# Performance work log

Measured on AMD Instinct MI355X. Metric: run time of the kernel, lower is better.

The kernel has to match this reference:

```python
import jax, jax.numpy as jnp
import numpy as np

EPS = 1e-8


def setup_inputs() -> dict:
    key = jax.random.key(0)
    k1, k2, k3, k4, k5 = jax.random.split(key, 5)
    N, B, T, D = 8, 2, 2048, 2048
    F = 4 * D
    blocks = jax.random.normal(k1, (N, B, T, D), dtype=jnp.float32)
    partial_block = jax.random.normal(k2, (B, T, D), dtype=jnp.float32)
    proj_w = jax.random.normal(k3, (D,), dtype=jnp.float32) * 0.02
    norm_scale = jnp.ones((D,), dtype=jnp.float32)
    ffn_w1 = jax.random.normal(k4, (D, F), dtype=jnp.float32) * 0.02
    ffn_w2 = jax.random.normal(k5, (F, D), dtype=jnp.float32) * 0.02
    return {
        "blocks": blocks,
        "partial_block": partial_block,
        "proj_w": proj_w,
        "norm_scale": norm_scale,
        "ffn_w1": ffn_w1,
        "ffn_w2": ffn_w2,
    }


def reference(blocks, partial_block, proj_w, norm_scale, ffn_w1, ffn_w2):
    # Stack completed blocks with current partial sum: V [N1, B, T, D]
    V = jnp.concatenate([blocks, partial_block[None]], axis=0)
    # RMSNorm over D (keys)
    rms = jnp.sqrt(jnp.mean(V * V, axis=-1, keepdims=True) + EPS)
    K = norm_scale * V / rms
    # Pseudo-query dot-product logits [N1, B, T], softmax over blocks (axis 0)
    logits = jnp.einsum('nbtd,d->nbt', K, proj_w)
    alpha = jax.nn.softmax(logits, axis=0)
    # Weighted sum of raw values -> new hidden state h [B, T, D]
    h = jnp.einsum('nbt,nbtd->btd', alpha, V)
    # Sublayer: standard FFN (D -> 4D gelu -> D)
    f_out = jax.nn.gelu(h @ ffn_w1) @ ffn_w2
    # layer_number % block_size != 0 branch: accumulate partial sum
    new_partial = partial_block + f_out
    return h, new_partial
```

## Files before the change

### kernel.cpp

```cpp
#include <hip/hip_runtime.h>

typedef unsigned short ushort_t;
typedef __bf16 bf16x8 __attribute__((ext_vector_type(8)));
typedef float f32x4 __attribute__((ext_vector_type(4)));

#define NB 8
#define BB 2
#define TT 2048
#define DD 2048
#define FF 8192
#define MM (BB * TT)
#define BTD ((size_t)BB * TT * DD)

__device__ __forceinline__ unsigned short f2bf(float f) {
  unsigned int u = __float_as_uint(f);
  u += 0x7FFFu + ((u >> 16) & 1u);
  return (unsigned short)(u >> 16);
}

__device__ __forceinline__ float gelu_tanh(float x) {
  float u = 0.7978845608028654f * (x + 0.044715f * x * x * x);
  float e = __expf(2.0f * u);
  float th = 1.0f - 2.0f / (e + 1.0f);
  return 0.5f * x * (1.0f + th);
}

template <int N>
__device__ __forceinline__ void wait_vmcnt() {
  if constexpr (N == 0) asm volatile("s_waitcnt vmcnt(0)" ::: "memory");
  else if constexpr (N == 2) asm volatile("s_waitcnt vmcnt(2)" ::: "memory");
  else if constexpr (N == 4) asm volatile("s_waitcnt vmcnt(4)" ::: "memory");
  else if constexpr (N == 6) asm volatile("s_waitcnt vmcnt(6)" ::: "memory");
}

#define ASYNC_COPY16(gp, lp)                                                   \
  __builtin_amdgcn_global_load_lds(                                            \
      (__attribute__((address_space(1))) void*)(gp),                           \
      (__attribute__((address_space(3))) void*)(lp), 16, 0, 0)

__global__ __launch_bounds__(256) void transpose_conv(
    const float* __restrict__ in, ushort_t* __restrict__ out, int R, int C) {
  __shared__ float tile[32][33];
  const int tx = threadIdx.x & 31, ty = threadIdx.x >> 5;
  const int r0 = blockIdx.y * 32, c0 = blockIdx.x * 32;
#pragma unroll
  for (int i = 0; i < 32; i += 8)
    tile[ty + i][tx] = in[(size_t)(r0 + ty + i) * C + (c0 + tx)];
  __syncthreads();
#pragma unroll
  for (int i = 0; i < 32; i += 8)
    out[(size_t)(c0 + ty + i) * R + (r0 + tx)] = f2bf(tile[tx][ty + i]);
}

__global__ __launch_bounds__(256) void attn_fuse(
    const float* __restrict__ blocks, const float* __restrict__ partial,
    const float* __restrict__ proj_w, const float* __restrict__ norm_scale,
    float* __restrict__ h_out, ushort_t* __restrict__ h_bf) {
  const int t = threadIdx.x;
  const int bt = blockIdx.x;
  const size_t rowoff = (size_t)bt * DD;
  const int d0 = t * 4;

  float w[8];
  {
    float4 ns = *(const float4*)(norm_scale + d0);
    float4 pw = *(const float4*)(proj_w + d0);
    w[0] = ns.x * pw.x; w[1] = ns.y * pw.y; w[2] = ns.z * pw.z; w[3] = ns.w * pw.w;
    ns = *(const float4*)(norm_scale + 1024 + d0);
    pw = *(const float4*)(proj_w + 1024 + d0);
    w[4] = ns.x * pw.x; w[5] = ns.y * pw.y; w[6] = ns.z * pw.z; w[7] = ns.w * pw.w;
  }

  float ss[9], dt[9];
#pragma unroll
  for (int n = 0; n < 9; ++n) {
    const float* rp = (n < 8) ? (blocks + (size_t)n * BTD + rowoff)
                              : (partial + rowoff);
    float4 v0 = *(const float4*)(rp + d0);
    float4 v1 = *(const float4*)(rp + 1024 + d0);
    ss[n] = v0.x * v0.x + v0.y * v0.y + v0.z * v0.z + v0.w * v0.w +
            v1.x * v1.x + v1.y * v1.y + v1.z * v1.z + v1.w * v1.w;
    dt[n] = v0.x * w[0] + v0.y * w[1] + v0.z * w[2] + v0.w * w[3] +
            v1.x * w[4] + v1.y * w[5] + v1.z * w[6] + v1.w * w[7];
  }

  __shared__ float red[2][9][4];
  const int lane = t & 63, wv = t >> 6;
#pragma unroll
  for (int n = 0; n < 9; ++n) {
    float a = ss[n], c = dt[n];
#pragma unroll
    for (int off = 32; off > 0; off >>= 1) {
      a += __shfl_down(a, off, 64);
      c += __shfl_down(c, off, 64);
    }
    if (lane == 0) { red[0][n][wv] = a; red[1][n][wv] = c; }
  }
  __syncthreads();
  __shared__ float logit_s[9];
  if (t < 9) {
    float a = red[0][t][0] + red[0][t][1] + red[0][t][2] + red[0][t][3];
    float c = red[1][t][0] + red[1][t][1] + red[1][t][2] + red[1][t][3];
    logit_s[t] = c * rsqrtf(a * (1.0f / (float)DD) + 1e-8f);
  }
  __syncthreads();

  float lg[9], mx = -1e30f;
#pragma unroll
  for (int n = 0; n < 9; ++n) { lg[n] = logit_s[n]; mx = fmaxf(mx, lg[n]); }
  float den = 0.0f;
#pragma unroll
  for (int n = 0; n < 9; ++n) { lg[n] = __expf(lg[n] - mx); den += lg[n]; }
  const float inv = 1.0f / den;

  float h[8] = {0, 0, 0, 0, 0, 0, 0, 0};
#pragma unroll
  for (int n = 0; n < 9; ++n) {
    const float* rp = (n < 8) ? (blocks + (size_t)n * BTD + rowoff)
                              : (partial + rowoff);
    float4 v0 = *(const float4*)(rp + d0);
    float4 v1 = *(const float4*)(rp + 1024 + d0);
    const float a = lg[n] * inv;
    h[0] += a * v0.x; h[1] += a * v0.y; h[2] += a * v0.z; h[3] += a * v0.w;
    h[4] += a * v1.x; h[5] += a * v1.y; h[6] += a * v1.z; h[7] += a * v1.w;
  }

  float4 o0 = {h[0], h[1], h[2], h[3]}, o1 = {h[4], h[5], h[6], h[7]};
  *(float4*)(h_out + rowoff + d0) = o0;
  *(float4*)(h_out + rowoff + 1024 + d0) = o1;
  uint2 p0, p1;
  p0.x = (unsigned)f2bf(h[0]) | ((unsigned)f2bf(h[1]) << 16);
  p0.y = (unsigned)f2bf(h[2]) | ((unsigned)f2bf(h[3]) << 16);
  p1.x = (unsigned)f2bf(h[4]) | ((unsigned)f2bf(h[5]) << 16);
  p1.y = (unsigned)f2bf(h[6]) | ((unsigned)f2bf(h[7]) << 16);
  *(uint2*)(h_bf + rowoff + d0) = p0;
  *(uint2*)(h_bf + rowoff + 1024 + d0) = p1;
}

template <int BN, int EPI>
__global__ __launch_bounds__(512) void gemm256(
    const ushort_t* __restrict__ A, const ushort_t* __restrict__ BT,
    const int K, const int N, const int GX, ushort_t* __restrict__ Cb,
    const float* __restrict__ addend, float* __restrict__ Cf) {
  constexpr int BM = 256;
  constexpr int WCN = BN / 4;
  constexpr int MF = 8;
  constexpr int NF = WCN / 16;
  constexpr int NH = NF / 2;
  constexpr int NCB = BN / 64;
  constexpr int AUS = BM * 64;
  constexpr int WP2 = (BN == 256) ? 6 : 4;

  __shared__ __align__(16) ushort_t lds0[(BM + BN) * 64];
  __shared__ __align__(16) ushort_t lds1[(BM + BN) * 64];

  const int t = threadIdx.x;
  const int lane = t & 63, wv = t >> 6;
  const int wr = wv >> 2, wc = wv & 3;
  const int fr = lane & 15;

  const int nwg = gridDim.x;
  const int wg = blockIdx.x;
  const int swz = (wg & 7) * (nwg >> 3) + (wg >> 3);
  const int bx = swz % GX, by = swz / GX;
  const int row0 = by * BM, col0 = bx * BN;

  const int sr = t >> 3;
  const int scolb = ((t & 7) * 16) ^ ((sr & 7) << 4);
  const ushort_t* gA = A + (size_t)(row0 + sr) * K + (scolb >> 1);
  const ushort_t* gB = BT + (size_t)(col0 + sr) * K + (scolb >> 1);

#define STAGE_A(W, c, KT)                                                      \
  ASYNC_COPY16(gA + (size_t)((c)*64) * K + (KT)*64, &W[(c)*4096 + wv * 512])
#define STAGE_B(W, c, KT)                                                      \
  ASYNC_COPY16(gB + (size_t)((c)*64) * K + (KT)*64,                            \
               &W[AUS + (c)*4096 + wv * 512])

  const int s_lane = (fr & 7) << 4;
  const int offk0 = ((lane >> 4) * 16) ^ s_lane;
  const int offk1 = (64 + (lane >> 4) * 16) ^ s_lane;
  const int aoffA = (wr * 128 + fr) * 128;
  int boffB[NF];
#pragma unroll
  for (int n = 0; n < NF; ++n)
    boffB[n] = AUS * 2 + (wc * WCN + n * 16 + fr) * 128;

  f32x4 acc[MF][NF];
#pragma unroll
  for (int m = 0; m < MF; ++m)
#pragma unroll
    for (int n = 0; n < NF; ++n) {
      f32x4 z = {0.f, 0.f, 0.f, 0.f};
      acc[m][n] = z;
    }

#define MFMA_(a, b, c) __builtin_amdgcn_mfma_f32_16x16x32_bf16(a, b, c, 0, 0, 0)

#define TILE(Rb, Wb, KT, S)                                                    \
  {                                                                            \
    const char* _L = (const char*)Rb;                                          \
    bf16x8 af[4][2], b0[NH][2], b1[NH][2];                                     \
                                                 \
    _Pragma("unroll") for (int m = 0; m < 4; ++m) {                            \
      af[m][0] = *(const bf16x8*)(_L + aoffA + m * 2048 + offk0);              \
      af[m][1] = *(const bf16x8*)(_L + aoffA + m * 2048 + offk1);              \
    }                                                                          \
    _Pragma("unroll") for (int n = 0; n < NH; ++n) {                           \
      b0[n][0] = *(const bf16x8*)(_L + boffB[n] + offk0);                      \
      b0[n][1] = *(const bf16x8*)(_L + boffB[n] + offk1);                      \
    }                                                                          \
    if (S) {                                                                   \
      STAGE_A(Wb, 0, KT); STAGE_A(Wb, 2, KT);                                  \
      STAGE_B(Wb, 0, KT); STAGE_B(Wb, 1, KT);                                  \
    }                                                                          \
    __builtin_amdgcn_s_barrier();                                              \
    __builtin_amdgcn_s_setprio(1);                                             \
    _Pragma("unroll") for (int m = 0; m < 4; ++m)                              \
      _Pragma("unroll") for (int n = 0; n < NH; ++n) {                         \
        acc[m][n] = MFMA_(af[m][0], b0[n][0], acc[m][n]);                      \
        acc[m][n] = MFMA_(af[m][1], b0[n][1], acc[m][n]);                      \
      }                                                                        \
    __builtin_amdgcn_s_setprio(0);                                             \
    __builtin_amdgcn_s_barrier();                                              \
                                                 \
    _Pragma("unroll") for (int n = 0; n < NH; ++n) {                           \
      b1[n][0] = *(const bf16x8*)(_L + boffB[NH + n] + offk0);                 \
      b1[n][1] = *(const bf16x8*)(_L + boffB[NH + n] + offk1);                 \
    }                                                                          \
    if (S && BN == 256) { STAGE_B(Wb, 2, KT); STAGE_B(Wb, 3, KT); }            \
    __builtin_amdgcn_s_barrier();                                              \
    __builtin_amdgcn_s_setprio(1);                                             \
    _Pragma("unroll") for (int m = 0; m < 4; ++m)                              \
      _Pragma("unroll") for (int n = 0; n < NH; ++n) {                         \
        acc[m][NH + n] = MFMA_(af[m][0], b1[n][0], acc[m][NH + n]);            \
        acc[m][NH + n] = MFMA_(af[m][1], b1[n][1], acc[m][NH + n]);            \
      }                                                                        \
    __builtin_amdgcn_s_setprio(0);                                             \
    if (S) wait_vmcnt<WP2>(); else wait_vmcnt<0>();                            \
    __builtin_amdgcn_s_barrier();                                              \
                                                 \
    _Pragma("unroll") for (int m = 0; m < 4; ++m) {                            \
      af[m][0] = *(const bf16x8*)(_L + aoffA + (4 + m) * 2048 + offk0);        \
      af[m][1] = *(const bf16x8*)(_L + aoffA + (4 + m) * 2048 + offk1);        \
    }                                                                          \
    if (S) { STAGE_A(Wb, 1, KT); STAGE_A(Wb, 3, KT); }                         \
    __builtin_amdgcn_s_barrier();                                              \
    __builtin_amdgcn_s_setprio(1);                                             \
    _Pragma("unroll") for (int m = 0; m < 4; ++m)                              \
      _Pragma("unroll") for (int n = 0; n < NH; ++n) {                         \
        acc[4 + m][NH + n] = MFMA_(af[m][0], b1[n][0], acc[4 + m][NH + n]);    \
        acc[4 + m][NH + n] = MFMA_(af[m][1], b1[n][1], acc[4 + m][NH + n]);    \
      }                                                                        \
    __builtin_amdgcn_s_setprio(0);                                             \
    __builtin_amdgcn_s_barrier();                                              \
                                  \
    _Pragma("unroll") for (int n = 0; n < NH; ++n) {                           \
      b0[n][0] = *(const bf16x8*)(_L + boffB[n] + offk0);                      \
      b0[n][1] = *(const bf16x8*)(_L + boffB[n] + offk1);                      \
    }                                                                          \
    __builtin_amdgcn_s_barrier();                                              \
    __builtin_amdgcn_s_setprio(1);                                             \
    _Pragma("unroll") for (int m = 0; m < 4; ++m)                              \
      _Pragma("unroll") for (int n = 0; n < NH; ++n) {                         \
        acc[4 + m][n] = MFMA_(af[m][0], b0[n][0], acc[4 + m][n]);              \
        acc[4 + m][n] = MFMA_(af[m][1], b0[n][1], acc[4 + m][n]);              \
      }                                                                        \
    __builtin_amdgcn_s_setprio(0);                                             \
    if (S) wait_vmcnt<2>();                                                    \
    __builtin_amdgcn_s_barrier();                                              \
  }

  STAGE_A(lds0, 0, 0); STAGE_A(lds0, 2, 0);
  STAGE_B(lds0, 0, 0); STAGE_B(lds0, 1, 0);
  if (BN == 256) { STAGE_B(lds0, 2, 0); STAGE_B(lds0, 3, 0); }
  STAGE_A(lds0, 1, 0); STAGE_A(lds0, 3, 0);
  wait_vmcnt<2>();
  __builtin_amdgcn_s_barrier();

  const int NT = K >> 6;
  for (int kt = 0; kt < NT; kt += 2) {
    TILE(lds0, lds1, kt + 1, (kt + 1) < NT);
    TILE(lds1, lds0, kt + 2, (kt + 2) < NT);
  }

  const int r4 = (lane >> 4) * 4;
#pragma unroll
  for (int m = 0; m < MF; ++m) {
    const int grow = row0 + wr * 128 + m * 16 + r4;
#pragma unroll
    for (int n = 0; n < NF; ++n) {
      const int gcol = col0 + wc * WCN + n * 16 + fr;
#pragma unroll
      for (int r = 0; r < 4; ++r) {
        const float v = acc[m][n][r];
        const size_t idx = (size_t)(grow + r) * N + gcol;
        if (EPI == 0) {
          Cb[idx] = f2bf(gelu_tanh(v));
        } else {
          Cf[idx] = v + addend[idx];
        }
      }
    }
  }
#undef TILE
#undef MFMA_
#undef STAGE_A
#undef STAGE_B
}

extern "C" void kernel_launch(void* const* d_in, const int* in_sizes, int n_in,
                              void* d_out, int out_size, void* d_ws,
                              size_t ws_size, hipStream_t stream) {
  const float* blocks = (const float*)d_in[0];
  const float* partial = (const float*)d_in[1];
  const float* proj_w = (const float*)d_in[2];
  const float* norm_scale = (const float*)d_in[3];
  const float* w1 = (const float*)d_in[4];
  const float* w2 = (const float*)d_in[5];

  float* out = (float*)d_out;
  float* h_out = out;
  float* new_partial = out + BTD;

  char* ws = (char*)d_ws;
  ushort_t* h_bf = (ushort_t*)ws;
  ushort_t* w1T = (ushort_t*)(ws + (size_t)16777216);
  ushort_t* w2T = (ushort_t*)(ws + (size_t)16777216 + 33554432);
  ushort_t* act = (ushort_t*)(ws + (size_t)16777216 + 2 * 33554432ull);

  transpose_conv<<<dim3(FF / 32, DD / 32), 256, 0, stream>>>(w1, w1T, DD, FF);
  transpose_conv<<<dim3(DD / 32, FF / 32), 256, 0, stream>>>(w2, w2T, FF, DD);

  attn_fuse<<<MM, 256, 0, stream>>>(blocks, partial, proj_w, norm_scale, h_out,
                                    h_bf);

  gemm256<256, 0><<<(FF / 256) * (MM / 256), 512, 0, stream>>>(
      h_bf, w1T, DD, FF, FF / 256, act, nullptr, nullptr);
  gemm256<128, 1><<<(DD / 128) * (MM / 256), 512, 0, stream>>>(
      act, w2T, FF, DD, DD / 128, nullptr, partial, new_partial);
}
```

Before: 426.9 us.

## Restructure GEMM main loop to prefetch next tile's A fragments across stages

Rewrites the GEMM inner pipeline so each K-tile step reads all B fragments at once, keeps two A-fragment register sets, and loads the next tile's first A half from the other LDS buffer while the current tile's last MFMA quads run. Async global-to-LDS staging is rescheduled across the two buffers with different vmcnt waits, and launch bounds now request two workgroups per CU. The aim is to hide LDS read latency behind MFMA work and raise occupancy. In exchange, register pressure rises (more live fragments under a tighter register cap), which may cause spills, and the new buffer-reuse ordering depends on the wait counts being correct.

Result: slower. 542.7 us (+27.1%).

```diff
diff --git a/kernel.cpp b/kernel.cpp
--- a/kernel.cpp
+++ b/kernel.cpp
@@ -138,7 +138,7 @@
 }
 
 template <int BN, int EPI>
-__global__ __launch_bounds__(512) void gemm256(
+__global__ __launch_bounds__(512, 2) void gemm256(
     const ushort_t* __restrict__ A, const ushort_t* __restrict__ BT,
     const int K, const int N, const int GX, ushort_t* __restrict__ Cb,
     const float* __restrict__ addend, float* __restrict__ Cf) {
@@ -149,7 +149,7 @@
   constexpr int NH = NF / 2;
   constexpr int NCB = BN / 64;
   constexpr int AUS = BM * 64;
-  constexpr int WP2 = (BN == 256) ? 6 : 4;
+  constexpr int W12 = (BN == 256) ? 6 : 4;
 
   __shared__ __align__(16) ushort_t lds0[(BM + BN) * 64];
   __shared__ __align__(16) ushort_t lds1[(BM + BN) * 64];
@@ -170,11 +170,16 @@
   const ushort_t* gA = A + (size_t)(row0 + sr) * K + (scolb >> 1);
   const ushort_t* gB = BT + (size_t)(col0 + sr) * K + (scolb >> 1);
 
-#define STAGE_A(W, c, KT)                                                      \
+#define ST_A(W, c, KT)                                                         \
   ASYNC_COPY16(gA + (size_t)((c)*64) * K + (KT)*64, &W[(c)*4096 + wv * 512])
-#define STAGE_B(W, c, KT)                                                      \
+#define ST_B(W, c, KT)                                                         \
   ASYNC_COPY16(gB + (size_t)((c)*64) * K + (KT)*64,                            \
                &W[AUS + (c)*4096 + wv * 512])
+#define STAGE_A02(W, KT) { ST_A(W, 0, KT); ST_A(W, 2, KT); }
+#define STAGE_A13(W, KT) { ST_A(W, 1, KT); ST_A(W, 3, KT); }
+#define STAGE_BB(W, KT)                                                        \
+  { ST_B(W, 0, KT); ST_B(W, 1, KT);                                            \
+    if (NCB == 4) { ST_B(W, 2, KT); ST_B(W, 3, KT); } }
 
   const int s_lane = (fr & 7) << 4;
   const int offk0 = ((lane >> 4) * 16) ^ s_lane;
@@ -185,102 +190,94 @@
   for (int n = 0; n < NF; ++n)
     boffB[n] = AUS * 2 + (wc * WCN + n * 16 + fr) * 128;
 
+  bf16x8 af0[4][2], af1[4][2], bfr[NF][2];
+
+#define READ_AF0(Lb)                                                           \
+  _Pragma("unroll") for (int m = 0; m < 4; ++m) {                              \
+    af0[m][0] = *(const bf16x8*)((const char*)(Lb) + aoffA + m * 2048 + offk0);\
+    af0[m][1] = *(const bf16x8*)((const char*)(Lb) + aoffA + m * 2048 + offk1);\
+  }
+#define READ_AF1(Lb)                                                           \
+  _Pragma("unroll") for (int m = 0; m < 4; ++m) {                              \
+    af1[m][0] =                                                                \
+        *(const bf16x8*)((const char*)(Lb) + aoffA + (4 + m) * 2048 + offk0);  \
+    af1[m][1] =                                                                \
+        *(const bf16x8*)((const char*)(Lb) + aoffA + (4 + m) * 2048 + offk1);  \
+  }
+#define READ_B(Lb)                                                             \
+  _Pragma("unroll") for (int n = 0; n < NF; ++n) {                             \
+    bfr[n][0] = *(const bf16x8*)((const char*)(Lb) + boffB[n] + offk0);        \
+    bfr[n][1] = *(const bf16x8*)((const char*)(Lb) + boffB[n] + offk1);        \
+  }
+
   f32x4 acc[MF][NF];
 #pragma unroll
-  for (int m = 0; m < MF; ++m)
+  for (int m = 0; m < 4; ++m)
 #pragma unroll
     for (int n = 0; n < NF; ++n) {
       f32x4 z = {0.f, 0.f, 0.f, 0.f};
-      acc[m][n] = z;
+      acc[m][n] = z; acc[4 + m][n] = z;
     }
 
 #define MFMA_(a, b, c) __builtin_amdgcn_mfma_f32_16x16x32_bf16(a, b, c, 0, 0, 0)
-
-#define TILE(Rb, Wb, KT, S)                                                    \
+#define QUAD(AF, MO, NO)                                                       \
+  _Pragma("unroll") for (int ks = 0; ks < 2; ++ks)                             \
+    _Pragma("unroll") for (int m = 0; m < 4; ++m)                              \
+      _Pragma("unroll") for (int n = 0; n < NH; ++n)                           \
+        acc[MO + m][NO + n] =                                                  \
+            MFMA_(AF[m][ks], bfr[NO + n][ks], acc[MO + m][NO + n]);
+
+#define HALF(Rb, Ob, T)                                                        \
   {                                                                            \
-    const char* _L = (const char*)Rb;                                          \
-    bf16x8 af[4][2], b0[NH][2], b1[NH][2];                                     \
-                                                 \
-    _Pragma("unroll") for (int m = 0; m < 4; ++m) {                            \
-      af[m][0] = *(const bf16x8*)(_L + aoffA + m * 2048 + offk0);              \
-      af[m][1] = *(const bf16x8*)(_L + aoffA + m * 2048 + offk1);              \
-    }                                                                          \
-    _Pragma("unroll") for (int n = 0; n < NH; ++n) {                           \
-      b0[n][0] = *(const bf16x8*)(_L + boffB[n] + offk0);                      \
-      b0[n][1] = *(const bf16x8*)(_L + boffB[n] + offk1);                      \
-    }                                                                          \
-    if (S) {                                                                   \
-      STAGE_A(Wb, 0, KT); STAGE_A(Wb, 2, KT);                                  \
-      STAGE_B(Wb, 0, KT); STAGE_B(Wb, 1, KT);                                  \
-    }                                                                          \
+    const bool s1 = (T) + 1 < NT, s2 = (T) + 2 < NT;                           \
+                           \
+    READ_B(Rb);                                                                \
+    if (s1) STAGE_BB(Ob, (T) + 1);                                             \
     __builtin_amdgcn_s_barrier();                                              \
     __builtin_amdgcn_s_setprio(1);                                             \
-    _Pragma("unroll") for (int m = 0; m < 4; ++m)                              \
-      _Pragma("unroll") for (int n = 0; n < NH; ++n) {                         \
-        acc[m][n] = MFMA_(af[m][0], b0[n][0], acc[m][n]);                      \
-        acc[m][n] = MFMA_(af[m][1], b0[n][1], acc[m][n]);                      \
-      }                                                                        \
+    QUAD(af0, 0, 0);                                                           \
     __builtin_amdgcn_s_setprio(0);                                             \
-    __builtin_amdgcn_s_barrier();                                              \
-                                                 \
-    _Pragma("unroll") for (int n = 0; n < NH; ++n) {                           \
-      b1[n][0] = *(const bf16x8*)(_L + boffB[NH + n] + offk0);                 \
-      b1[n][1] = *(const bf16x8*)(_L + boffB[NH + n] + offk1);                 \
-    }                                                                          \
-    if (S && BN == 256) { STAGE_B(Wb, 2, KT); STAGE_B(Wb, 3, KT); }            \
+    wait_vmcnt<W12>();                                                         \
+    __builtin_amdgcn_s_barrier();                                              \
+                     \
+    READ_AF1(Rb);                                                              \
+    if (s1) STAGE_A13(Ob, (T) + 1);                                            \
     __builtin_amdgcn_s_barrier();                                              \
     __builtin_amdgcn_s_setprio(1);                                             \
-    _Pragma("unroll") for (int m = 0; m < 4; ++m)                              \
-      _Pragma("unroll") for (int n = 0; n < NH; ++n) {                         \
-        acc[m][NH + n] = MFMA_(af[m][0], b1[n][0], acc[m][NH + n]);            \
-        acc[m][NH + n] = MFMA_(af[m][1], b1[n][1], acc[m][NH + n]);            \
-      }                                                                        \
+    QUAD(af0, 0, NH);                                                          \
     __builtin_amdgcn_s_setprio(0);                                             \
-    if (S) wait_vmcnt<WP2>(); else wait_vmcnt<0>();                            \
-    __builtin_amdgcn_s_barrier();                                              \
-                                                 \
-    _Pragma("unroll") for (int m = 0; m < 4; ++m) {                            \
-      af[m][0] = *(const bf16x8*)(_L + aoffA + (4 + m) * 2048 + offk0);        \
-      af[m][1] = *(const bf16x8*)(_L + aoffA + (4 + m) * 2048 + offk1);        \
-    }                                                                          \
-    if (S) { STAGE_A(Wb, 1, KT); STAGE_A(Wb, 3, KT); }                         \
+    wait_vmcnt<W12>();                                                         \
+    __builtin_amdgcn_s_barrier();                                              \
+            \
+    READ_AF0(Ob);                                                              \
+    if (s2) STAGE_A02(Rb, (T) + 2);                                            \
     __builtin_amdgcn_s_barrier();                                              \
     __builtin_amdgcn_s_setprio(1);                                             \
-    _Pragma("unroll") for (int m = 0; m < 4; ++m)                              \
-      _Pragma("unroll") for (int n = 0; n < NH; ++n) {                         \
-        acc[4 + m][NH + n] = MFMA_(af[m][0], b1[n][0], acc[4 + m][NH + n]);    \
-        acc[4 + m][NH + n] = MFMA_(af[m][1], b1[n][1], acc[4 + m][NH + n]);    \
-      }                                                                        \
+    QUAD(af1, 4, NH);                                                          \
     __builtin_amdgcn_s_setprio(0);                                             \
     __builtin_amdgcn_s_barrier();                                              \
-                                  \
-    _Pragma("unroll") for (int n = 0; n < NH; ++n) {                           \
-      b0[n][0] = *(const bf16x8*)(_L + boffB[n] + offk0);                      \
-      b0[n][1] = *(const bf16x8*)(_L + boffB[n] + offk1);                      \
-    }                                                                          \
+                                             \
     __builtin_amdgcn_s_barrier();                                              \
     __builtin_amdgcn_s_setprio(1);                                             \
-    _Pragma("unroll") for (int m = 0; m < 4; ++m)                              \
-      _Pragma("unroll") for (int n = 0; n < NH; ++n) {                         \
-        acc[4 + m][n] = MFMA_(af[m][0], b0[n][0], acc[4 + m][n]);              \
-        acc[4 + m][n] = MFMA_(af[m][1], b0[n][1], acc[4 + m][n]);              \
-      }                                                                        \
+    QUAD(af1, 4, 0);                                                           \
     __builtin_amdgcn_s_setprio(0);                                             \
-    if (S) wait_vmcnt<2>();                                                    \
-    __builtin_amdgcn_s_barrier();                                              \
-  }
-
-  STAGE_A(lds0, 0, 0); STAGE_A(lds0, 2, 0);
-  STAGE_B(lds0, 0, 0); STAGE_B(lds0, 1, 0);
-  if (BN == 256) { STAGE_B(lds0, 2, 0); STAGE_B(lds0, 3, 0); }
-  STAGE_A(lds0, 1, 0); STAGE_A(lds0, 3, 0);
+    wait_vmcnt<4>();                                                           \
+    __builtin_amdgcn_s_barrier();                                              \
+  }
+
+  const int NT = K >> 6;
+
+  STAGE_A02(lds0, 0);
+  STAGE_BB(lds0, 0);
+  STAGE_A13(lds0, 0);
+  STAGE_A02(lds1, 1);
   wait_vmcnt<2>();
   __builtin_amdgcn_s_barrier();
-
-  const int NT = K >> 6;
+  READ_AF0(lds0);
+
   for (int kt = 0; kt < NT; kt += 2) {
-    TILE(lds0, lds1, kt + 1, (kt + 1) < NT);
-    TILE(lds1, lds0, kt + 2, (kt + 2) < NT);
+    HALF(lds0, lds1, kt);
+    HALF(lds1, lds0, kt + 1);
   }
 
   const int r4 = (lane >> 4) * 4;
@@ -302,10 +299,17 @@
       }
     }
   }
-#undef TILE
+#undef HALF
+#undef QUAD
 #undef MFMA_
-#undef STAGE_A
-#undef STAGE_B
+#undef READ_AF0
+#undef READ_AF1
+#undef READ_B
+#undef STAGE_A02
+#undef STAGE_A13
+#undef STAGE_BB
+#undef ST_A
+#undef ST_B
 }
 
 extern "C" void kernel_launch(void* const* d_in, const int* in_sizes, int n_in,
```
